# Optimization experiments

Measured on AMD Instinct MI355X. Metric: run time of the kernel, lower is better.

## Reference

```python
import jax, jax.numpy as jnp
import numpy as np

B, S, D, H = 4, 1024, 1024, 16
HD = D // H
EPS = 1e-5


def setup_inputs() -> dict:
    key = jax.random.key(0)
    ks = jax.random.split(key, 12)
    sc = 0.02
    return {
        "x": jax.random.normal(ks[0], (B, S, D), jnp.float32),
        "WQ": jax.random.normal(ks[1], (D, D), jnp.float32) * sc,
        "WK": jax.random.normal(ks[2], (D, D), jnp.float32) * sc,
        "WV": jax.random.normal(ks[3], (D, D), jnp.float32) * sc,
        "Wo": jax.random.normal(ks[4], (D, D), jnp.float32) * sc,
        "bo": jnp.zeros((D,), jnp.float32),
        "W1": jax.random.normal(ks[5], (D, 4 * D), jnp.float32) * sc,
        "b1": jnp.zeros((4 * D,), jnp.float32),
        "W2": jax.random.normal(ks[6], (4 * D, D), jnp.float32) * sc,
        "b2": jnp.zeros((D,), jnp.float32),
        "ln1_s": jnp.ones((D,), jnp.float32),
        "ln1_b": jnp.zeros((D,), jnp.float32),
        "ln2_s": jnp.ones((D,), jnp.float32),
        "ln2_b": jnp.zeros((D,), jnp.float32),
    }


def _layernorm(x, scale, shift):
    mean = jnp.mean(x, axis=-1, keepdims=True)
    var = jnp.mean((x - mean) ** 2, axis=-1, keepdims=True)  # unbiased=False
    return scale * ((x - mean) / jnp.sqrt(var + EPS)) + shift


def _gelu(x):
    c = jnp.sqrt(2.0 / jnp.pi).astype(x.dtype)
    return 0.5 * x * (1.0 + jnp.tanh(c * (x + 0.044715 * x ** 3)))


def reference(x, WQ, WK, WV, Wo, bo, W1, b1, W2, b2, ln1_s, ln1_b, ln2_s, ln2_b):
    b, s, d = x.shape
    # --- attention sub-block (pre-norm) ---
    h = _layernorm(x, ln1_s, ln1_b)
    q = (h @ WQ).reshape(b, s, H, HD).transpose(0, 2, 1, 3)  # [B,H,S,HD]
    k = (h @ WK).reshape(b, s, H, HD).transpose(0, 2, 1, 3)
    v = (h @ WV).reshape(b, s, H, HD).transpose(0, 2, 1, 3)
    scores = jnp.einsum("bhqd,bhkd->bhqk", q, k)
    causal = jnp.triu(jnp.ones((s, s), dtype=bool), k=1)
    scores = jnp.where(causal, -jnp.inf, scores)
    attn = jax.nn.softmax(scores / jnp.sqrt(jnp.float32(HD)), axis=-1)
    ctx = jnp.einsum("bhqk,bhkd->bhqd", attn, v)
    ctx = ctx.transpose(0, 2, 1, 3).reshape(b, s, d)
    x = x + (ctx @ Wo + bo)
    # --- FF sub-block (pre-norm) ---
    h = _layernorm(x, ln2_s, ln2_b)
    h = _gelu(h @ W1 + b1)
    return x + (h @ W2 + b2)
```

## Files before the change

kernel.cpp:

```cpp
#include <hip/hip_runtime.h>
#include <hip/hip_bf16.h>

#define DIM   1024
#define NHEAD 16
#define HDIM  64
#define BATCH 4
#define SEQ   1024
#define MTOT  (BATCH*SEQ)
#define DFF   (4*DIM)
#define LDQ   3072

typedef _Float16 f16x8 __attribute__((ext_vector_type(8)));
typedef _Float16 f16x4 __attribute__((ext_vector_type(4)));
typedef float    f32x4 __attribute__((ext_vector_type(4)));

__device__ __forceinline__ float geluf(float x) {
    float z2 = 1.5957691216057308f * (x + 0.044715f * x * x * x);
    return x * __builtin_amdgcn_rcpf(1.0f + __expf(-z2));
}

__device__ __forceinline__ int swz_off(int row, int slot) {
    return row * 128 + ((slot ^ (row & 7)) << 4);
}
__device__ __forceinline__ f16x8 ldsfrag(const _Float16* s, int row, int slot) {
    return *(const f16x8*)((const char*)s + swz_off(row, slot));
}

template <int NCHUNK>
__device__ __forceinline__ void stage_async(const _Float16* __restrict__ g, int ld,
                                            _Float16* s, int w, int lane) {
    int r_in = lane >> 3;
    int sslot = lane & 7;
    int lslot = sslot ^ r_in;
#pragma unroll
    for (int q = 0; q < NCHUNK; ++q) {
        int chunk = w * NCHUNK + q;
        int row = chunk * 8 + r_in;
        const _Float16* gp = g + (size_t)row * ld + lslot * 8;
        _Float16* sp = s + chunk * 512;
        __builtin_amdgcn_global_load_lds(
            (const __attribute__((address_space(1))) void*)gp,
            (__attribute__((address_space(3))) void*)sp, 16, 0, 0);
    }
}

__global__ __launch_bounds__(256) void k_tcvt(const float* __restrict__ src,
                                              _Float16* __restrict__ dst,
                                              int K, int N) {
    __shared__ float tile[32][33];
    int n0 = blockIdx.x * 32, k0 = blockIdx.y * 32;
    int tx = threadIdx.x, ty = threadIdx.y;
#pragma unroll
    for (int i = 0; i < 32; i += 8)
        tile[ty + i][tx] = src[(size_t)(k0 + ty + i) * N + (n0 + tx)];
    __syncthreads();
#pragma unroll
    for (int i = 0; i < 32; i += 8)
        dst[(size_t)(n0 + ty + i) * K + (k0 + tx)] = (_Float16)tile[tx][ty + i];
}

__global__ __launch_bounds__(256) void k_tcvt4(const float* __restrict__ s0,
                                               const float* __restrict__ s1,
                                               const float* __restrict__ s2,
                                               const float* __restrict__ s3,
                                               _Float16* __restrict__ dst) {
    __shared__ float tile[32][33];
    const float* src = blockIdx.z == 0 ? s0 : (blockIdx.z == 1 ? s1 :
                       (blockIdx.z == 2 ? s2 : s3));
    _Float16* d = dst + (size_t)blockIdx.z * (1024 * 1024);
    int n0 = blockIdx.x * 32, k0 = blockIdx.y * 32;
    int tx = threadIdx.x, ty = threadIdx.y;
#pragma unroll
    for (int i = 0; i < 32; i += 8)
        tile[ty + i][tx] = src[(size_t)(k0 + ty + i) * 1024 + (n0 + tx)];
    __syncthreads();
#pragma unroll
    for (int i = 0; i < 32; i += 8)
        d[(size_t)(n0 + ty + i) * 1024 + (k0 + tx)] = (_Float16)tile[tx][ty + i];
}

__global__ __launch_bounds__(256) void k_ln(const float* __restrict__ x,
                                            const float* __restrict__ sc,
                                            const float* __restrict__ sh,
                                            _Float16* __restrict__ out) {
    int row = blockIdx.x;
    int t = threadIdx.x;
    float4 v = ((const float4*)(x + (size_t)row * DIM))[t];
    float sum = v.x + v.y + v.z + v.w;
    float sq  = v.x * v.x + v.y * v.y + v.z * v.z + v.w * v.w;
#pragma unroll
    for (int m = 1; m < 64; m <<= 1) {
        sum += __shfl_xor(sum, m);
        sq  += __shfl_xor(sq, m);
    }
    __shared__ float rs[4], rq[4];
    int w = t >> 6;
    if ((t & 63) == 0) { rs[w] = sum; rq[w] = sq; }
    __syncthreads();
    sum = rs[0] + rs[1] + rs[2] + rs[3];
    sq  = rq[0] + rq[1] + rq[2] + rq[3];
    float mean = sum * (1.0f / DIM);
    float var  = sq * (1.0f / DIM) - mean * mean;
    float rstd = rsqrtf(var + 1e-5f);
    float4 s4 = ((const float4*)sc)[t];
    float4 b4 = ((const float4*)sh)[t];
    f16x4 o;
    o[0] = (_Float16)(s4.x * ((v.x - mean) * rstd) + b4.x);
    o[1] = (_Float16)(s4.y * ((v.y - mean) * rstd) + b4.y);
    o[2] = (_Float16)(s4.z * ((v.z - mean) * rstd) + b4.z);
    o[3] = (_Float16)(s4.w * ((v.w - mean) * rstd) + b4.w);
    ((f16x4*)(out + (size_t)row * DIM))[t] = o;
}

template <int EPI>
__global__ __launch_bounds__(256) void k_gemm(const _Float16* __restrict__ A,
                                              const _Float16* __restrict__ BT,
                                              int N, int K, int gx,
                                              _Float16* __restrict__ Ch,
                                              const float* __restrict__ bias) {
    __shared__ _Float16 As[2][128 * 64];
    __shared__ _Float16 Bs[2][128 * 64];
    int t = threadIdx.x;
    int bid = blockIdx.x;
    int lin = (bid & 7) * ((int)gridDim.x >> 3) + (bid >> 3);
    int m0 = (lin / gx) * 128, n0 = (lin % gx) * 128;
    int lane = t & 63, w = t >> 6;
    int wm = (w >> 1) * 64, wn = (w & 1) * 64;
    int lr = lane & 15, lg = lane >> 4;
    f32x4 acc[4][4];
#pragma unroll
    for (int i = 0; i < 4; ++i)
#pragma unroll
        for (int j = 0; j < 4; ++j) acc[i][j] = (f32x4){0.f, 0.f, 0.f, 0.f};

    const _Float16* Ag = A  + (size_t)m0 * K;
    const _Float16* Bg = BT + (size_t)n0 * K;
    int nt = K / 64;
    stage_async<4>(Ag, K, As[0], w, lane);
    stage_async<4>(Bg, K, Bs[0], w, lane);
    for (int tt = 0; tt < nt; ++tt) {
        int cur = tt & 1, nxt = cur ^ 1;
        if (tt + 1 < nt) {
            stage_async<4>(Ag + (tt + 1) * 64, K, As[nxt], w, lane);
            stage_async<4>(Bg + (tt + 1) * 64, K, Bs[nxt], w, lane);
            asm volatile("s_waitcnt vmcnt(8)" ::: "memory");
        } else {
            asm volatile("s_waitcnt vmcnt(0)" ::: "memory");
        }
        __builtin_amdgcn_sched_barrier(0);
        __builtin_amdgcn_s_barrier();
        __builtin_amdgcn_sched_barrier(0);
#pragma unroll
        for (int kk = 0; kk < 2; ++kk) {
            f16x8 a[4], b[4];
#pragma unroll
            for (int i = 0; i < 4; ++i) a[i] = ldsfrag(As[cur], wm + i * 16 + lr, kk * 4 + lg);
#pragma unroll
            for (int j = 0; j < 4; ++j) b[j] = ldsfrag(Bs[cur], wn + j * 16 + lr, kk * 4 + lg);
            __builtin_amdgcn_s_setprio(1);
#pragma unroll
            for (int i = 0; i < 4; ++i)
#pragma unroll
                for (int j = 0; j < 4; ++j)
                    acc[i][j] = __builtin_amdgcn_mfma_f32_16x16x32_f16(a[i], b[j], acc[i][j], 0, 0, 0);
            __builtin_amdgcn_s_setprio(0);
        }
        __builtin_amdgcn_s_barrier();
    }
#pragma unroll
    for (int i = 0; i < 4; ++i) {
#pragma unroll
        for (int j = 0; j < 4; ++j) {
            int row = m0 + wm + i * 16 + lg * 4;
            int col = n0 + wn + j * 16 + lr;
#pragma unroll
            for (int r = 0; r < 4; ++r) {
                float v = acc[i][j][r];
                size_t idx = (size_t)(row + r) * N + col;
                if constexpr (EPI == 0) Ch[idx] = (_Float16)v;
                else                    Ch[idx] = (_Float16)geluf(v + bias[col]);
            }
        }
    }
}

__global__ __launch_bounds__(256) void k_gemm64(const _Float16* __restrict__ A,
                                                const _Float16* __restrict__ BT,
                                                int N, int K,
                                                float* __restrict__ Cf,
                                                const float* __restrict__ bias,
                                                const float* __restrict__ resid) {
    __shared__ _Float16 As[3][128 * 64];
    __shared__ _Float16 Bs[3][64 * 64];
    int t = threadIdx.x;
    int bid = blockIdx.x;
    int lin = (bid & 7) * ((int)gridDim.x >> 3) + (bid >> 3);
    int gx = N / 64;
    int m0 = (lin / gx) * 128, n0 = (lin % gx) * 64;
    int lane = t & 63, w = t >> 6;
    int wm = w * 32;
    int lr = lane & 15, lg = lane >> 4;
    f32x4 acc[2][4];
#pragma unroll
    for (int i = 0; i < 2; ++i)
#pragma unroll
        for (int j = 0; j < 4; ++j) acc[i][j] = (f32x4){0.f, 0.f, 0.f, 0.f};

    const _Float16* Ag = A  + (size_t)m0 * K;
    const _Float16* Bg = BT + (size_t)n0 * K;
    int nt = K / 64;
    stage_async<4>(Ag, K, As[0], w, lane);
    stage_async<2>(Bg, K, Bs[0], w, lane);
    stage_async<4>(Ag + 64, K, As[1], w, lane);
    stage_async<2>(Bg + 64, K, Bs[1], w, lane);
    for (int tt = 0; tt < nt; ++tt) {
        if (tt + 1 < nt) asm volatile("s_waitcnt vmcnt(6)" ::: "memory");
        else             asm volatile("s_waitcnt vmcnt(0)" ::: "memory");
        __builtin_amdgcn_sched_barrier(0);
        __builtin_amdgcn_s_barrier();
        __builtin_amdgcn_sched_barrier(0);
        const _Float16* Ac = As[tt % 3];
        const _Float16* Bc = Bs[tt % 3];
#pragma unroll
        for (int kk = 0; kk < 2; ++kk) {
            f16x8 a[2], b[4];
#pragma unroll
            for (int i = 0; i < 2; ++i) a[i] = ldsfrag(Ac, wm + i * 16 + lr, kk * 4 + lg);
#pragma unroll
            for (int j = 0; j < 4; ++j) b[j] = ldsfrag(Bc, j * 16 + lr, kk * 4 + lg);
            __builtin_amdgcn_s_setprio(1);
#pragma unroll
            for (int i = 0; i < 2; ++i)
#pragma unroll
                for (int j = 0; j < 4; ++j)
                    acc[i][j] = __builtin_amdgcn_mfma_f32_16x16x32_f16(a[i], b[j], acc[i][j], 0, 0, 0);
            __builtin_amdgcn_s_setprio(0);
        }
        if (tt + 2 < nt) {
            int nb = (tt + 2) % 3;
            stage_async<4>(Ag + (tt + 2) * 64, K, As[nb], w, lane);
            stage_async<2>(Bg + (tt + 2) * 64, K, Bs[nb], w, lane);
        }
    }
#pragma unroll
    for (int i = 0; i < 2; ++i) {
#pragma unroll
        for (int j = 0; j < 4; ++j) {
            int row = m0 + wm + i * 16 + lg * 4;
            int col = n0 + j * 16 + lr;
#pragma unroll
            for (int r = 0; r < 4; ++r) {
                size_t idx = (size_t)(row + r) * N + col;
                Cf[idx] = acc[i][j][r] + bias[col] + resid[idx];
            }
        }
    }
}

__device__ __forceinline__ void load_k(const _Float16* __restrict__ QKV,
                                       size_t base, int k0, int ck,
                                       int lr, int lg, f16x8 (&kr)[2][4]) {
#pragma unroll
    for (int kk = 0; kk < 2; ++kk)
#pragma unroll
        for (int j = 0; j < 4; ++j)
            kr[kk][j] = *(const f16x8*)(QKV + (base + k0 + j * 16 + lr) * LDQ + ck + kk * 32 + lg * 8);
}

__device__ __forceinline__ void attn_tile_sw(const _Float16* __restrict__ QKV,
                                             const f16x8 (&bk)[2][4],
                                             f16x8 (&knext)[2][4], bool pf, int k0next,
                                             const f16x8 (&aq)[2][2],
                                             f32x4 (&cacc)[2][4],
                                             float (&mrun)[2], float (&lrun)[2],
                                             _Float16* Ps,
                                             size_t base, int ck, int cv,
                                             int k0, int q0, bool diag,
                                             int lr, int lg) {
    f32x4 sacc[2][4];
#pragma unroll
    for (int i = 0; i < 2; ++i)
#pragma unroll
        for (int j = 0; j < 4; ++j) sacc[i][j] = (f32x4){0.f, 0.f, 0.f, 0.f};
    __builtin_amdgcn_s_setprio(1);
#pragma unroll
    for (int kk = 0; kk < 2; ++kk)
#pragma unroll
        for (int i = 0; i < 2; ++i)
#pragma unroll
            for (int j = 0; j < 4; ++j)
                sacc[i][j] = __builtin_amdgcn_mfma_f32_16x16x32_f16(bk[kk][j], aq[i][kk], sacc[i][j], 0, 0, 0);
    __builtin_amdgcn_s_setprio(0);
    if (pf) load_k(QKV, base, k0next, ck, lr, lg, knext);
    if (diag) {
#pragma unroll
        for (int i = 0; i < 2; ++i) {
            int qq = q0 + i * 16 + lr;
#pragma unroll
            for (int j = 0; j < 4; ++j)
#pragma unroll
                for (int r = 0; r < 4; ++r) {
                    int kc = k0 + j * 16 + lg * 4 + r;
                    if (kc > qq) sacc[i][j][r] = -1e30f;
                }
        }
    }
#pragma unroll
    for (int i = 0; i < 2; ++i) {
        float tm = -1e30f;
#pragma unroll
        for (int j = 0; j < 4; ++j)
#pragma unroll
            for (int r = 0; r < 4; ++r) tm = fmaxf(tm, sacc[i][j][r]);
        tm = fmaxf(tm, __shfl_xor(tm, 16));
        tm = fmaxf(tm, __shfl_xor(tm, 32));
        float m2 = fmaxf(mrun[i], tm);
        float al = __expf(mrun[i] - m2);
        mrun[i] = m2;
#pragma unroll
        for (int jd = 0; jd < 4; ++jd)
#pragma unroll
            for (int r = 0; r < 4; ++r) cacc[i][jd][r] *= al;
        float ps = 0.f;
#pragma unroll
        for (int j = 0; j < 4; ++j)
#pragma unroll
            for (int r = 0; r < 4; ++r) {
                float p = __expf(sacc[i][j][r] - m2);
                sacc[i][j][r] = p;
                ps += p;
            }
        ps += __shfl_xor(ps, 16);
        ps += __shfl_xor(ps, 32);
        lrun[i] = lrun[i] * al + ps;
    }
#pragma unroll
    for (int i = 0; i < 2; ++i) {
        int q = i * 16 + lr;
#pragma unroll
        for (int j = 0; j < 4; ++j) {
            int kc0 = j * 16 + lg * 4;
            int ks = kc0 >> 3;
            f16x4 pv4;
#pragma unroll
            for (int r = 0; r < 4; ++r) pv4[r] = (_Float16)sacc[i][j][r];
            *(f16x4*)((char*)Ps + q * 128 + ((ks ^ (q & 7)) << 4) + (kc0 & 7) * 2) = pv4;
        }
    }
    const _Float16* vb = QKV + (base + k0) * LDQ + cv;
#pragma unroll
    for (int kk = 0; kk < 2; ++kk) {
        f16x8 pa[2], bv[4];
#pragma unroll
        for (int i = 0; i < 2; ++i) pa[i] = ldsfrag(Ps, i * 16 + lr, kk * 4 + lg);
        const _Float16* vk = vb + (size_t)(kk * 32 + lg * 8) * LDQ + lr;
#pragma unroll
        for (int jd = 0; jd < 4; ++jd)
#pragma unroll
            for (int e = 0; e < 8; ++e)
                bv[jd][e] = vk[(size_t)e * LDQ + jd * 16];
        __builtin_amdgcn_s_setprio(1);
#pragma unroll
        for (int i = 0; i < 2; ++i)
#pragma unroll
            for (int jd = 0; jd < 4; ++jd)
                cacc[i][jd] = __builtin_amdgcn_mfma_f32_16x16x32_f16(bv[jd], pa[i], cacc[i][jd], 0, 0, 0);
        __builtin_amdgcn_s_setprio(0);
    }
}

__global__ __launch_bounds__(64) void k_attn(const _Float16* __restrict__ QKV,
                                             _Float16* __restrict__ Og) {
    __shared__ _Float16 Ps[32 * 64];
    int lane = threadIdx.x;
    int id = blockIdx.x;
    int bh = id & 63;
    int qt = (SEQ / 32 - 1) - (id >> 6);
    int h = bh & 15, b = bh >> 4;
    int q0 = qt * 32;
    int lr = lane & 15, lg = lane >> 4;
    size_t base = (size_t)b * SEQ;
    int cq = h * HDIM, ck = 1024 + h * HDIM, cv = 2048 + h * HDIM;

    f16x8 aq[2][2];
#pragma unroll
    for (int i = 0; i < 2; ++i)
#pragma unroll
        for (int kk = 0; kk < 2; ++kk) {
            f16x8 v = *(const f16x8*)(QKV + (base + q0 + i * 16 + lr) * LDQ + cq + kk * 32 + lg * 8);
#pragma unroll
            for (int e = 0; e < 8; ++e) v[e] = v[e] * (_Float16)0.125f;
            aq[i][kk] = v;
        }

    f32x4 cacc[2][4];
#pragma unroll
    for (int i = 0; i < 2; ++i)
#pragma unroll
        for (int j = 0; j < 4; ++j) cacc[i][j] = (f32x4){0.f, 0.f, 0.f, 0.f};
    float mrun[2], lrun[2];
#pragma unroll
    for (int i = 0; i < 2; ++i) { mrun[i] = -1e30f; lrun[i] = 0.f; }

    int ntiles = q0 / 64 + 1;
    f16x8 kA[2][4], kB[2][4];
    load_k(QKV, base, 0, ck, lr, lg, kA);
    for (int kt = 0; kt < ntiles; kt += 2) {
        attn_tile_sw(QKV, kA, kB, kt + 1 < ntiles, (kt + 1) * 64,
                     aq, cacc, mrun, lrun, Ps, base, ck, cv,
                     kt * 64, q0, kt == ntiles - 1, lr, lg);
        if (kt + 1 >= ntiles) break;
        attn_tile_sw(QKV, kB, kA, kt + 2 < ntiles, (kt + 2) * 64,
                     aq, cacc, mrun, lrun, Ps, base, ck, cv,
                     (kt + 1) * 64, q0, kt + 1 == ntiles - 1, lr, lg);
    }
#pragma unroll
    for (int i = 0; i < 2; ++i) {
        float rl = 1.0f / lrun[i];
        int qq = q0 + i * 16 + lr;
#pragma unroll
        for (int jd = 0; jd < 4; ++jd) {
            f16x4 o4;
#pragma unroll
            for (int r = 0; r < 4; ++r) o4[r] = (_Float16)(cacc[i][jd][r] * rl);
            *(f16x4*)(Og + (base + qq) * DIM + h * HDIM + jd * 16 + lg * 4) = o4;
        }
    }
}

extern "C" void kernel_launch(void* const* d_in, const int* in_sizes, int n_in,
                              void* d_out, int out_size, void* d_ws, size_t ws_size,
                              hipStream_t stream) {
    const float* x    = (const float*)d_in[0];
    const float* WQ   = (const float*)d_in[1];
    const float* WK   = (const float*)d_in[2];
    const float* WV   = (const float*)d_in[3];
    const float* Wo   = (const float*)d_in[4];
    const float* bo   = (const float*)d_in[5];
    const float* W1   = (const float*)d_in[6];
    const float* b1   = (const float*)d_in[7];
    const float* W2   = (const float*)d_in[8];
    const float* b2   = (const float*)d_in[9];
    const float* ln1s = (const float*)d_in[10];
    const float* ln1b = (const float*)d_in[11];
    const float* ln2s = (const float*)d_in[12];
    const float* ln2b = (const float*)d_in[13];
    float* out = (float*)d_out;
    char* ws = (char*)d_ws;
    const size_t MB = 1024 * 1024;
    _Float16* WTqkv = (_Float16*)(ws + 0 * MB);
    _Float16* WTo   = (_Float16*)(ws + 6 * MB);
    _Float16* WT1   = (_Float16*)(ws + 8 * MB);
    _Float16* WT2   = (_Float16*)(ws + 16 * MB);
    _Float16* h1    = (_Float16*)(ws + 24 * MB);
    _Float16* qkvb  = (_Float16*)(ws + 32 * MB);
    _Float16* ctx   = (_Float16*)(ws + 56 * MB);
    _Float16* h2    = (_Float16*)(ws + 64 * MB);
    _Float16* ff1   = (_Float16*)(ws + 72 * MB);
    float*    x2    = (float*)   (ws + 104 * MB);

    dim3 tb(32, 8);
    k_tcvt4<<<dim3(32, 32, 4), tb, 0, stream>>>(WQ, WK, WV, Wo, WTqkv);
    k_tcvt<<<dim3(128, 32), tb, 0, stream>>>(W1, WT1, 1024, 4096);
    k_tcvt<<<dim3(32, 128), tb, 0, stream>>>(W2, WT2, 4096, 1024);

    k_ln<<<MTOT, 256, 0, stream>>>(x, ln1s, ln1b, h1);

    k_gemm<0><<<dim3(768), 256, 0, stream>>>(h1, WTqkv, LDQ, DIM, 24, qkvb, nullptr);

    k_attn<<<dim3(2048), 64, 0, stream>>>(qkvb, ctx);

    k_gemm64<<<dim3(512), 256, 0, stream>>>(ctx, WTo, DIM, DIM, x2, bo, x);

    k_ln<<<MTOT, 256, 0, stream>>>(x2, ln2s, ln2b, h2);

    k_gemm<1><<<dim3(1024), 256, 0, stream>>>(h2, WT1, DFF, DIM, 32, ff1, b1);

    k_gemm64<<<dim3(512), 256, 0, stream>>>(ff1, WT2, DIM, DFF, out, b2, x2);
}
```

Before: 218.5 us.

## Split-K the FF2 GEMM with 128x128 tiles and a separate reduction kernel

Replaces the 128x64-tile FF2 GEMM, which has a long K=4096 loop, with a 2-way split-K kernel on 128x128 tiles. Each half writes fp32 partials into workspace, and a new elementwise kernel sums the two partials and adds bias and residual. The larger tiles improve operand reuse while keeping 512 blocks in flight. The cost is writing and re-reading two 16 MB fp32 partial buffers plus one extra kernel launch.

```diff
diff --git a/kernel.cpp b/kernel.cpp
--- a/kernel.cpp
+++ b/kernel.cpp
@@ -182,6 +182,92 @@
             }
         }
     }
+}
+
+__global__ __launch_bounds__(256) void k_gemmSK(const _Float16* __restrict__ A,
+                                                const _Float16* __restrict__ BT,
+                                                float* __restrict__ Part) {
+    __shared__ _Float16 As[2][128 * 64];
+    __shared__ _Float16 Bs[2][128 * 64];
+    const int N = 1024, K = DFF, KH = DFF / 2;
+    int t = threadIdx.x;
+    int bid = blockIdx.x;
+    int lin = (bid & 7) * ((int)gridDim.x >> 3) + (bid >> 3);
+    int ks = lin & 1;
+    int t2 = lin >> 1;
+    int m0 = (t2 >> 3) * 128, n0 = (t2 & 7) * 128;
+    int lane = t & 63, w = t >> 6;
+    int wm = (w >> 1) * 64, wn = (w & 1) * 64;
+    int lr = lane & 15, lg = lane >> 4;
+    f32x4 acc[4][4];
+#pragma unroll
+    for (int i = 0; i < 4; ++i)
+#pragma unroll
+        for (int j = 0; j < 4; ++j) acc[i][j] = (f32x4){0.f, 0.f, 0.f, 0.f};
+
+    const _Float16* Ag = A  + (size_t)m0 * K + ks * KH;
+    const _Float16* Bg = BT + (size_t)n0 * K + ks * KH;
+    float* P = Part + (size_t)ks * MTOT * N;
+    int nt = KH / 64;
+    stage_async<4>(Ag, K, As[0], w, lane);
+    stage_async<4>(Bg, K, Bs[0], w, lane);
+    for (int tt = 0; tt < nt; ++tt) {
+        int cur = tt & 1, nxt = cur ^ 1;
+        if (tt + 1 < nt) {
+            stage_async<4>(Ag + (tt + 1) * 64, K, As[nxt], w, lane);
+            stage_async<4>(Bg + (tt + 1) * 64, K, Bs[nxt], w, lane);
+            asm volatile("s_waitcnt vmcnt(8)" ::: "memory");
+        } else {
+            asm volatile("s_waitcnt vmcnt(0)" ::: "memory");
+        }
+        __builtin_amdgcn_sched_barrier(0);
+        __builtin_amdgcn_s_barrier();
+        __builtin_amdgcn_sched_barrier(0);
+#pragma unroll
+        for (int kk = 0; kk < 2; ++kk) {
+            f16x8 a[4], b[4];
+#pragma unroll
+            for (int i = 0; i < 4; ++i) a[i] = ldsfrag(As[cur], wm + i * 16 + lr, kk * 4 + lg);
+#pragma unroll
+            for (int j = 0; j < 4; ++j) b[j] = ldsfrag(Bs[cur], wn + j * 16 + lr, kk * 4 + lg);
+            __builtin_amdgcn_s_setprio(1);
+#pragma unroll
+            for (int i = 0; i < 4; ++i)
+#pragma unroll
+                for (int j = 0; j < 4; ++j)
+                    acc[i][j] = __builtin_amdgcn_mfma_f32_16x16x32_f16(a[i], b[j], acc[i][j], 0, 0, 0);
+            __builtin_amdgcn_s_setprio(0);
+        }
+        __builtin_amdgcn_s_barrier();
+    }
+#pragma unroll
+    for (int i = 0; i < 4; ++i)
+#pragma unroll
+        for (int j = 0; j < 4; ++j) {
+            int row = m0 + wm + i * 16 + lg * 4;
+            int col = n0 + wn + j * 16 + lr;
+#pragma unroll
+            for (int r = 0; r < 4; ++r)
+                P[(size_t)(row + r) * N + col] = acc[i][j][r];
+        }
+}
+
+__global__ __launch_bounds__(256) void k_red(const float* __restrict__ p0,
+                                             const float* __restrict__ p1,
+                                             const float* __restrict__ bias,
+                                             const float* __restrict__ resid,
+                                             float* __restrict__ out) {
+    int i4 = blockIdx.x * 256 + threadIdx.x;
+    float4 a = ((const float4*)p0)[i4];
+    float4 b = ((const float4*)p1)[i4];
+    float4 r = ((const float4*)resid)[i4];
+    float4 bs = ((const float4*)bias)[i4 & 255];
+    float4 o;
+    o.x = a.x + b.x + r.x + bs.x;
+    o.y = a.y + b.y + r.y + bs.y;
+    o.z = a.z + b.z + r.z + bs.z;
+    o.w = a.w + b.w + r.w + bs.w;
+    ((float4*)out)[i4] = o;
 }
 
 __global__ __launch_bounds__(256) void k_gemm64(const _Float16* __restrict__ A,
@@ -458,6 +544,7 @@
     _Float16* h2    = (_Float16*)(ws + 64 * MB);
     _Float16* ff1   = (_Float16*)(ws + 72 * MB);
     float*    x2    = (float*)   (ws + 104 * MB);
+    float*    part  = (float*)   (ws + 24 * MB);
 
     dim3 tb(32, 8);
     k_tcvt4<<<dim3(32, 32, 4), tb, 0, stream>>>(WQ, WK, WV, Wo, WTqkv);
@@ -476,5 +563,7 @@
 
     k_gemm<1><<<dim3(1024), 256, 0, stream>>>(h2, WT1, DFF, DIM, 32, ff1, b1);
 
-    k_gemm64<<<dim3(512), 256, 0, stream>>>(ff1, WT2, DIM, DFF, out, b2, x2);
-}
+    k_gemmSK<<<dim3(512), 256, 0, stream>>>(ff1, WT2, part);
+    k_red<<<dim3(MTOT * DIM / 4 / 256), 256, 0, stream>>>(
+        part, part + (size_t)MTOT * DIM, b2, x2, out);
+}
```

After: 219.4 us. Within noise of the previous version (+0.4%).

## Add dedicated 128x256 tile GEMM with K=32 double buffering for FF1

Applied to the files above, without the earlier changes.

Adds a specialized FF1 GEMM kernel that uses 128x256 output tiles with each wave computing 64x128, staging 32-wide K slices through a new 4-slot swizzled LDS layout with double buffering. It replaces the generic 1024-block GEMM launch with 512 larger blocks. The aim is higher arithmetic intensity per LDS and global load and fewer blocks. In exchange it raises register pressure (128 accumulator floats per lane) and may lower occupancy, and each K step is shorter, so barriers are more frequent relative to compute.

```diff
diff --git a/kernel.cpp b/kernel.cpp
--- a/kernel.cpp
+++ b/kernel.cpp
@@ -25,6 +25,12 @@
 __device__ __forceinline__ f16x8 ldsfrag(const _Float16* s, int row, int slot) {
     return *(const f16x8*)((const char*)s + swz_off(row, slot));
 }
+__device__ __forceinline__ int swz32_off(int row, int slot) {
+    return row * 64 + ((slot ^ (row & 3)) << 4);
+}
+__device__ __forceinline__ f16x8 ldsfrag32(const _Float16* s, int row, int slot) {
+    return *(const f16x8*)((const char*)s + swz32_off(row, slot));
+}
 
 template <int NCHUNK>
 __device__ __forceinline__ void stage_async(const _Float16* __restrict__ g, int ld,
@@ -36,6 +42,23 @@
     for (int q = 0; q < NCHUNK; ++q) {
         int chunk = w * NCHUNK + q;
         int row = chunk * 8 + r_in;
+        const _Float16* gp = g + (size_t)row * ld + lslot * 8;
+        _Float16* sp = s + chunk * 512;
+        __builtin_amdgcn_global_load_lds(
+            (const __attribute__((address_space(1))) void*)gp,
+            (__attribute__((address_space(3))) void*)sp, 16, 0, 0);
+    }
+}
+template <int NCHUNK>
+__device__ __forceinline__ void stage32_async(const _Float16* __restrict__ g, int ld,
+                                              _Float16* s, int w, int lane) {
+    int r_in = lane >> 2;
+    int sslot = lane & 3;
+    int lslot = sslot ^ (r_in & 3);
+#pragma unroll
+    for (int q = 0; q < NCHUNK; ++q) {
+        int chunk = w * NCHUNK + q;
+        int row = chunk * 16 + r_in;
         const _Float16* gp = g + (size_t)row * ld + lslot * 8;
         _Float16* sp = s + chunk * 512;
         __builtin_amdgcn_global_load_lds(
@@ -179,6 +202,74 @@
                 size_t idx = (size_t)(row + r) * N + col;
                 if constexpr (EPI == 0) Ch[idx] = (_Float16)v;
                 else                    Ch[idx] = (_Float16)geluf(v + bias[col]);
+            }
+        }
+    }
+}
+
+__global__ __launch_bounds__(256) void k_gemmF(const _Float16* __restrict__ A,
+                                               const _Float16* __restrict__ BT,
+                                               _Float16* __restrict__ Ch,
+                                               const float* __restrict__ bias) {
+    const int N = DFF, K = DIM;
+    __shared__ _Float16 As[2][128 * 32];
+    __shared__ _Float16 Bs[2][256 * 32];
+    int t = threadIdx.x;
+    int bid = blockIdx.x;
+    int lin = (bid & 7) * 64 + (bid >> 3);
+    int m0 = (lin >> 4) * 128, n0 = (lin & 15) * 256;
+    int lane = t & 63, w = t >> 6;
+    int wm = (w >> 1) * 64, wn = (w & 1) * 128;
+    int lr = lane & 15, lg = lane >> 4;
+    f32x4 acc[4][8];
+#pragma unroll
+    for (int i = 0; i < 4; ++i)
+#pragma unroll
+        for (int j = 0; j < 8; ++j) acc[i][j] = (f32x4){0.f, 0.f, 0.f, 0.f};
+
+    const _Float16* Ag = A  + (size_t)m0 * K;
+    const _Float16* Bg = BT + (size_t)n0 * K;
+    int nt = K / 32;
+    stage32_async<2>(Ag, K, As[0], w, lane);
+    stage32_async<4>(Bg, K, Bs[0], w, lane);
+    for (int tt = 0; tt < nt; ++tt) {
+        int cur = tt & 1, nxt = cur ^ 1;
+        if (tt + 1 < nt) {
+            stage32_async<2>(Ag + (tt + 1) * 32, K, As[nxt], w, lane);
+            stage32_async<4>(Bg + (tt + 1) * 32, K, Bs[nxt], w, lane);
+            asm volatile("s_waitcnt vmcnt(6)" ::: "memory");
+        } else {
+            asm volatile("s_waitcnt vmcnt(0)" ::: "memory");
+        }
+        __builtin_amdgcn_sched_barrier(0);
+        __builtin_amdgcn_s_barrier();
+        __builtin_amdgcn_sched_barrier(0);
+        {
+            f16x8 a[4], b[8];
+#pragma unroll
+            for (int i = 0; i < 4; ++i) a[i] = ldsfrag32(As[cur], wm + i * 16 + lr, lg);
+#pragma unroll
+            for (int j = 0; j < 8; ++j) b[j] = ldsfrag32(Bs[cur], wn + j * 16 + lr, lg);
+            __builtin_amdgcn_s_setprio(1);
+#pragma unroll
+            for (int i = 0; i < 4; ++i)
+#pragma unroll
+                for (int j = 0; j < 8; ++j)
+                    acc[i][j] = __builtin_amdgcn_mfma_f32_16x16x32_f16(a[i], b[j], acc[i][j], 0, 0, 0);
+            __builtin_amdgcn_s_setprio(0);
+        }
+        __builtin_amdgcn_s_barrier();
+    }
+#pragma unroll
+    for (int i = 0; i < 4; ++i) {
+#pragma unroll
+        for (int j = 0; j < 8; ++j) {
+            int row = m0 + wm + i * 16 + lg * 4;
+            int col = n0 + wn + j * 16 + lr;
+#pragma unroll
+            for (int r = 0; r < 4; ++r) {
+                size_t idx = (size_t)(row + r) * N + col;
+                Ch[idx] = (_Float16)geluf(acc[i][j][r] + bias[col]);
             }
         }
     }
@@ -474,7 +565,7 @@
 
     k_ln<<<MTOT, 256, 0, stream>>>(x2, ln2s, ln2b, h2);
 
-    k_gemm<1><<<dim3(1024), 256, 0, stream>>>(h2, WT1, DFF, DIM, 32, ff1, b1);
+    k_gemmF<<<dim3(512), 256, 0, stream>>>(h2, WT1, ff1, b1);
 
     k_gemm64<<<dim3(512), 256, 0, stream>>>(ff1, WT2, DIM, DFF, out, b2, x2);
 }
```

New measurement: 223.7 us. +2.4%, slower.
